# Kernel tuning notes

Measured on AMD Instinct MI355X. Metric: run time of the kernel, lower is better.

Reference implementation:

```python
import jax, jax.numpy as jnp
import numpy as np

N = 50000      # nodes
E = 800000     # edges
G = 512        # graphs
IN = 544; HID = 64; H = 4; OUT = 2
EPS = 1e-5

def setup_inputs():
    key = jax.random.key(0)
    ks = jax.random.split(key, 16)
    x = jax.random.normal(ks[0], (N, IN), jnp.float32)
    edge_index = jax.random.randint(ks[1], (2, E), 0, N, jnp.int64)
    batch = jnp.sort(jax.random.randint(ks[2], (N,), 0, G, jnp.int64))
    s = lambda k, shp, fan: jax.random.normal(k, shp, jnp.float32) / np.sqrt(fan)
    return {
        'x': x, 'edge_index': edge_index, 'batch': batch,
        'ln_g': jnp.ones((32,), jnp.float32), 'ln_b': jnp.zeros((32,), jnp.float32),
        'bn1_g': jnp.ones((512,), jnp.float32), 'bn1_b': jnp.zeros((512,), jnp.float32),
        'Wc': s(ks[3], (16, 512), 512), 'bc': jnp.zeros((16,), jnp.float32),
        'bn2_g': jnp.ones((48,), jnp.float32), 'bn2_b': jnp.zeros((48,), jnp.float32),
        'Wp': s(ks[4], (HID, 48), 48), 'bp': jnp.zeros((HID,), jnp.float32),
        'Wg': s(ks[5], (H * HID, HID), HID),
        'att_src': s(ks[6], (H, HID), HID), 'att_dst': s(ks[7], (H, HID), HID),
        'bg': jnp.zeros((H * HID,), jnp.float32),
        'bn3_g': jnp.ones((H * HID,), jnp.float32), 'bn3_b': jnp.zeros((H * HID,), jnp.float32),
        'W1': s(ks[8], (HID, H * HID), H * HID), 'b1': jnp.zeros((HID,), jnp.float32),
        'W2': s(ks[9], (OUT, HID), HID), 'b2': jnp.zeros((OUT,), jnp.float32),
    }

def _batchnorm(x, g, b):
    mu = jnp.mean(x, axis=0)
    var = jnp.var(x, axis=0)
    return (x - mu) * jax.lax.rsqrt(var + EPS) * g + b

def _forward(x, ln_g, ln_b, bn1_g, bn1_b, Wc, bc, bn2_g, bn2_b, Wp, bp,
             Wg, att_src, att_dst, bg, bn3_g, bn3_b, W1, b1, W2, b2,
             edge_index, batch):
    # feature split + norms
    x_cnn = _batchnorm(x[:, :512], bn1_g, bn1_b)
    f = x[:, 512:]
    mu = jnp.mean(f, axis=-1, keepdims=True)
    var = jnp.var(f, axis=-1, keepdims=True)
    f = (f - mu) * jax.lax.rsqrt(var + EPS) * ln_g + ln_b
    x_cnn = x_cnn @ Wc.T + bc                      # [N,16]
    z = jnp.concatenate([x_cnn, f], axis=1)        # [N,48]
    z = _batchnorm(z, bn2_g, bn2_b)
    z = jax.nn.relu(z @ Wp.T + bp)                 # [N,HID] (dropout=eval identity)
    # GATConv (concat=True, negative_slope=0.2)
    h = (z @ Wg.T).reshape(N, H, HID)              # [N,H,C]
    a_src = jnp.sum(h * att_src, axis=-1)          # [N,H]
    a_dst = jnp.sum(h * att_dst, axis=-1)          # [N,H]
    src, dst = edge_index[0], edge_index[1]
    e = jax.nn.leaky_relu(a_src[src] + a_dst[dst], 0.2)   # [E,H]
    m = jax.ops.segment_max(e, dst, num_segments=N)
    m = jnp.where(jnp.isfinite(m), m, 0.0)
    ex = jnp.exp(e - m[dst])
    s = jax.ops.segment_sum(ex, dst, num_segments=N)
    alpha = ex / jnp.maximum(s, 1e-16)[dst]               # [E,H]
    out = jax.ops.segment_sum(alpha[:, :, None] * h[src], dst, num_segments=N)
    out = out.reshape(N, H * HID) + bg
    # BatchNorm + ELU + mean pool + MLP head
    out = jax.nn.elu(_batchnorm(out, bn3_g, bn3_b))
    cnt = jax.ops.segment_sum(jnp.ones((N,), out.dtype), batch, num_segments=G)
    pooled = jax.ops.segment_sum(out, batch, num_segments=G) / jnp.maximum(cnt, 1.0)[:, None]
    hmlp = jax.nn.relu(pooled @ W1.T + b1)
    return hmlp @ W2.T + b2                        # [G,OUT]

def reference(x, edge_index, batch, ln_g, ln_b, bn1_g, bn1_b, Wc, bc, bn2_g, bn2_b,
              Wp, bp, Wg, att_src, att_dst, bg, bn3_g, bn3_b, W1, b1, W2, b2):
    return _forward(x, ln_g, ln_b, bn1_g, bn1_b, Wc, bc, bn2_g, bn2_b, Wp, bp,
                    Wg, att_src, att_dst, bg, bn3_g, bn3_b, W1, b1, W2, b2,
                    edge_index, batch)
```

## Files before the change

### kernel.cpp

```cpp
#include <hip/hip_runtime.h>

static constexpr int N_   = 50000;
static constexpr int E_   = 800000;
static constexpr int G_   = 512;
static constexpr int IN_  = 544;
static constexpr float EPS_ = 1e-5f;
static constexpr int NBLK = 782;

static constexpr int BN1C = 32;
static constexpr int BN3C = 16;
static constexpr int BN2C = 8;
static constexpr size_t OFF_BN1C   = 0;
static constexpr size_t OFF_BN2C   = 131072;
static constexpr size_t OFF_BN3C   = 134144;
static constexpr size_t ZERO_BYTES = 166912;
static constexpr size_t OFF_COUNT  = 166912;
static constexpr size_t OFF_OFFS   = 366912;
static constexpr size_t OFF_BH     = 566912;
static constexpr size_t OFF_BTOT   = 1367680;
static constexpr size_t OFF_BBASE  = 1368704;
static constexpr size_t OFF_SORTD  = 1369856;
static constexpr size_t OFF_SORTS  = 2969856;
static constexpr size_t OFF_SRCS   = 6169856;
static constexpr size_t OFF_WC2    = 9369856;
static constexpr size_t OFF_C2     = 9402624;
static constexpr size_t OFF_WP2    = 9402880;
static constexpr size_t OFF_CP     = 9415168;
static constexpr size_t OFF_WGT    = 9415424;
static constexpr size_t OFF_ASRC   = 9480960;
static constexpr size_t OFF_ADST   = 10280960;
static constexpr size_t OFF_Z      = 11080960;
static constexpr size_t OFF_H      = 20680960;
static constexpr size_t OFF_OUTP   = 46280960;

#define DEV static __device__ __forceinline__

DEV float lrelu(float v) { return v > 0.f ? v : 0.2f * v; }
DEV unsigned short f2bf(float f) {
    unsigned u = __float_as_uint(f);
    return (unsigned short)((u + 0x7fffu + ((u >> 16) & 1u)) >> 16);
}

__global__ __launch_bounds__(256) void k_bn1(
        const float* __restrict__ x, float* __restrict__ bn1c) {
    __shared__ float4 ta[256];
    __shared__ float4 tb[256];
    int t = threadIdx.x;
    int cq = t & 127, rsub = t >> 7;
    int c4 = cq << 2;
    float4 a = make_float4(0.f, 0.f, 0.f, 0.f);
    float4 b = make_float4(0.f, 0.f, 0.f, 0.f);
    for (int r = blockIdx.x * 2 + rsub; r < N_; r += gridDim.x * 2) {
        float4 v = *(const float4*)(x + (size_t)r * IN_ + c4);
        a.x += v.x; a.y += v.y; a.z += v.z; a.w += v.w;
        b.x += v.x * v.x; b.y += v.y * v.y; b.z += v.z * v.z; b.w += v.w * v.w;
    }
    ta[t] = a; tb[t] = b;
    __syncthreads();
    if (t < 128) {
        float4 sa = ta[t], sb = tb[t];
        float4 xa = ta[128 + t], xb = tb[128 + t];
        sa.x += xa.x; sa.y += xa.y; sa.z += xa.z; sa.w += xa.w;
        sb.x += xb.x; sb.y += xb.y; sb.z += xb.z; sb.w += xb.w;
        float* dst = bn1c + (size_t)(blockIdx.x & (BN1C - 1)) * 1024;
        int c = t << 2;
        atomicAdd(&dst[c + 0], sa.x); atomicAdd(&dst[c + 1], sa.y);
        atomicAdd(&dst[c + 2], sa.z); atomicAdd(&dst[c + 3], sa.w);
        atomicAdd(&dst[512 + c + 0], sb.x); atomicAdd(&dst[512 + c + 1], sb.y);
        atomicAdd(&dst[512 + c + 2], sb.z); atomicAdd(&dst[512 + c + 3], sb.w);
    }
}

__global__ __launch_bounds__(256) void k_rhist(
        const int* __restrict__ ei, int* __restrict__ blockhist) {
    __shared__ int hist[256];
    int t = threadIdx.x;
    hist[t] = 0;
    __syncthreads();
    int base = blockIdx.x * 1024;
#pragma unroll
    for (int k = 0; k < 4; k++) {
        int i = base + k * 256 + t;
        if (i < E_) atomicAdd(&hist[ei[E_ + i] >> 8], 1);
    }
    __syncthreads();
    blockhist[blockIdx.x * 256 + t] = hist[t];
}

__global__ __launch_bounds__(256) void k_rscan(
        int* __restrict__ blockhist, int* __restrict__ btot) {
    __shared__ int a[256];
    int b = blockIdx.x, t = threadIdx.x;
    int v[4]; int s = 0;
#pragma unroll
    for (int k = 0; k < 4; k++) {
        int j = t * 4 + k;
        v[k] = (j < NBLK) ? blockhist[j * 256 + b] : 0;
        s += v[k];
    }
    a[t] = s;
    for (int off = 1; off < 256; off <<= 1) {
        __syncthreads();
        int tmp = (t >= off) ? a[t - off] : 0;
        __syncthreads();
        a[t] += tmp;
    }
    __syncthreads();
    int run = a[t] - s;
#pragma unroll
    for (int k = 0; k < 4; k++) {
        int j = t * 4 + k;
        if (j < NBLK) { blockhist[j * 256 + b] = run; run += v[k]; }
    }
    if (t == 255) btot[b] = a[255];
}

__global__ __launch_bounds__(256) void k_rbase(
        const int* __restrict__ btot, int* __restrict__ bbase) {
    __shared__ int a[256];
    int t = threadIdx.x;
    int v = btot[t];
    a[t] = v;
    for (int off = 1; off < 256; off <<= 1) {
        __syncthreads();
        int tmp = (t >= off) ? a[t - off] : 0;
        __syncthreads();
        a[t] += tmp;
    }
    __syncthreads();
    bbase[t] = a[t] - v;
    if (t == 255) bbase[256] = a[255];
}

__global__ __launch_bounds__(256) void k_rscatter(
        const int* __restrict__ ei, const int* __restrict__ blockhist,
        const int* __restrict__ bbase, unsigned short* __restrict__ sortd,
        int* __restrict__ sorts) {
    __shared__ int cursor[256];
    int t = threadIdx.x;
    cursor[t] = bbase[t] + blockhist[blockIdx.x * 256 + t];
    __syncthreads();
    int base = blockIdx.x * 1024;
#pragma unroll
    for (int k = 0; k < 4; k++) {
        int i = base + k * 256 + t;
        if (i < E_) {
            int d = ei[E_ + i], s = ei[i];
            int pos = atomicAdd(&cursor[d >> 8], 1);
            sortd[pos] = (unsigned short)d;
            sorts[pos] = s;
        }
    }
}

__global__ __launch_bounds__(256) void k_rsort2(
        const unsigned short* __restrict__ sortd, const int* __restrict__ sorts,
        const int* __restrict__ bbase, int* __restrict__ count,
        int* __restrict__ offs, int* __restrict__ srcsort) {
    __shared__ int hist[256];
    __shared__ int pref[256];
    __shared__ int cursor[256];
    int b = blockIdx.x, t = threadIdx.x;
    int base = bbase[b], endp = bbase[b + 1];
    hist[t] = 0;
    __syncthreads();
    for (int i = base + t; i < endp; i += 256)
        atomicAdd(&hist[sortd[i] & 255], 1);
    __syncthreads();
    int hv = hist[t];
    pref[t] = hv;
    for (int off = 1; off < 256; off <<= 1) {
        __syncthreads();
        int tmp = (t >= off) ? pref[t - off] : 0;
        __syncthreads();
        pref[t] += tmp;
    }
    __syncthreads();
    int ex = pref[t] - hv;
    int idx = (b << 8) + t;
    if (idx < N_) { count[idx] = hv; offs[idx] = base + ex; }
    cursor[t] = ex;
    __syncthreads();
    for (int i = base + t; i < endp; i += 256) {
        int d = sortd[i], s = sorts[i];
        int pos = base + atomicAdd(&cursor[d & 255], 1);
        srcsort[pos] = s;
    }
}

__global__ __launch_bounds__(512) void k_fold1(
        const float* __restrict__ bn1c,
        const float* __restrict__ g, const float* __restrict__ b,
        const float* __restrict__ Wc, const float* __restrict__ bc,
        float* __restrict__ Wc2t, float* __restrict__ c2) {
    __shared__ float c2s[16];
    int j = threadIdx.x;
    if (j < 16) c2s[j] = 0.f;
    float sum = 0.f, sq = 0.f;
    for (int c = 0; c < BN1C; c++) {
        sum += bn1c[c * 1024 + j];
        sq  += bn1c[c * 1024 + 512 + j];
    }
    float mu  = sum / (float)N_;
    float var = sq / (float)N_ - mu * mu;
    float s   = g[j] * rsqrtf(var + EPS_);
    float tj  = b[j] - mu * s;
    __syncthreads();
    for (int i = 0; i < 16; i++) {
        float wv = Wc[i * 512 + j];
        Wc2t[i * 512 + j] = wv * s;
        float p = tj * wv;
        for (int m = 1; m < 64; m <<= 1) p += __shfl_xor(p, m);
        if ((j & 63) == 0) atomicAdd(&c2s[i], p);
    }
    __syncthreads();
    if (j < 16) c2[j] = c2s[j] + bc[j];
}

static constexpr int WSTRIDE = 516;
__global__ __launch_bounds__(512) void k_z(
        const float* __restrict__ x, const float* __restrict__ Wc2tg,
        const float* __restrict__ c2g, const float* __restrict__ lng,
        const float* __restrict__ lnb, float* __restrict__ z,
        float* __restrict__ bn2c) {
    __shared__ float wc2[16 * WSTRIDE];
    __shared__ float c2s[16];
    __shared__ float bsum[48];
    __shared__ float bsq[48];
    int t = threadIdx.x;
    for (int q = t; q < 8192; q += 512) {
        int row = q >> 9, col = q & 511;
        wc2[row * WSTRIDE + col] = Wc2tg[q];
    }
    if (t < 16) c2s[t] = c2g[t];
    if (t < 48) { bsum[t] = 0.f; bsq[t] = 0.f; }
    __syncthreads();
    int pr = t >> 3, i = t & 7;
    int n0 = blockIdx.x * 128 + pr * 2;
    int n1 = n0 + 1;
    bool v0 = n0 < N_, v1 = n1 < N_;
    const float4* xr0 = (const float4*)(x + (size_t)(v0 ? n0 : N_ - 1) * IN_);
    const float4* xr1 = (const float4*)(x + (size_t)(v1 ? n1 : N_ - 1) * IN_);
    const float4* w0 = (const float4*)(wc2 + i * WSTRIDE);
    const float4* w1 = (const float4*)(wc2 + (i + 8) * WSTRIDE);
    float a00 = c2s[i], a01 = c2s[i + 8];
    float a10 = a00, a11 = a01;
    for (int u = 0; u < 128; u++) {
        float4 xa = xr0[u], xb = xr1[u];
        float4 p = w0[u], q4 = w1[u];
        a00 += xa.x * p.x + xa.y * p.y + xa.z * p.z + xa.w * p.w;
        a01 += xa.x * q4.x + xa.y * q4.y + xa.z * q4.z + xa.w * q4.w;
        a10 += xb.x * p.x + xb.y * p.y + xb.z * p.z + xb.w * p.w;
        a11 += xb.x * q4.x + xb.y * q4.y + xb.z * q4.z + xb.w * q4.w;
    }
    float va[4], vb[4];
    float sm0 = 0.f, sq0 = 0.f, sm1 = 0.f, sq1 = 0.f;
#pragma unroll
    for (int jj = 0; jj < 4; jj++) {
        va[jj] = x[(size_t)(v0 ? n0 : N_ - 1) * IN_ + 512 + i + 8 * jj];
        vb[jj] = x[(size_t)(v1 ? n1 : N_ - 1) * IN_ + 512 + i + 8 * jj];
        sm0 += va[jj]; sq0 += va[jj] * va[jj];
        sm1 += vb[jj]; sq1 += vb[jj] * vb[jj];
    }
    for (int m = 1; m < 8; m <<= 1) {
        sm0 += __shfl_xor(sm0, m); sq0 += __shfl_xor(sq0, m);
        sm1 += __shfl_xor(sm1, m); sq1 += __shfl_xor(sq1, m);
    }
    float mu0 = sm0 * (1.f / 32.f), rs0 = rsqrtf(sq0 * (1.f / 32.f) - mu0 * mu0 + EPS_);
    float mu1 = sm1 * (1.f / 32.f), rs1 = rsqrtf(sq1 * (1.f / 32.f) - mu1 * mu1 + EPS_);
    float outa[6], outb[6];
    outa[0] = a00; outa[1] = a01; outb[0] = a10; outb[1] = a11;
#pragma unroll
    for (int jj = 0; jj < 4; jj++) {
        int c = i + 8 * jj;
        float gg = lng[c], bb = lnb[c];
        outa[2 + jj] = (va[jj] - mu0) * rs0 * gg + bb;
        outb[2 + jj] = (vb[jj] - mu1) * rs1 * gg + bb;
    }
    int cols[6] = { i, i + 8, 16 + i, 24 + i, 32 + i, 40 + i };
    if (v0) {
#pragma unroll
        for (int k = 0; k < 6; k++) z[n0 * 48 + cols[k]] = outa[k];
    }
    if (v1) {
#pragma unroll
        for (int k = 0; k < 6; k++) z[n1 * 48 + cols[k]] = outb[k];
    }
    float s6[6], q6[6];
#pragma unroll
    for (int k = 0; k < 6; k++) {
        float pa = v0 ? outa[k] : 0.f;
        float pb = v1 ? outb[k] : 0.f;
        s6[k] = pa + pb; q6[k] = pa * pa + pb * pb;
    }
#pragma unroll
    for (int m = 8; m < 64; m <<= 1) {
#pragma unroll
        for (int k = 0; k < 6; k++) {
            s6[k] += __shfl_xor(s6[k], m);
            q6[k] += __shfl_xor(q6[k], m);
        }
    }
    if ((t & 63) < 8) {
#pragma unroll
        for (int k = 0; k < 6; k++) {
            atomicAdd(&bsum[cols[k]], s6[k]);
            atomicAdd(&bsq[cols[k]],  q6[k]);
        }
    }
    __syncthreads();
    if (t < 48) {
        float* dst = bn2c + (size_t)(blockIdx.x & (BN2C - 1)) * 96;
        atomicAdd(&dst[t],      bsum[t]);
        atomicAdd(&dst[48 + t], bsq[t]);
    }
}

__global__ __launch_bounds__(256) void k_fold2_wgt(
        const float* __restrict__ bn2c,
        const float* __restrict__ g, const float* __restrict__ b,
        const float* __restrict__ Wp, const float* __restrict__ bp,
        float* __restrict__ Wp2, float* __restrict__ cp,
        const float* __restrict__ Wg, float* __restrict__ Wgt) {
    __shared__ float t2[48];
    int t = threadIdx.x;
    if (blockIdx.x > 0) {
        int idx = (blockIdx.x - 1) * 256 + t;
        int c = idx >> 6, k = idx & 63;
        Wgt[k * 256 + c] = Wg[idx];
        return;
    }
    if (t < 48) {
        float sum = 0.f, sq = 0.f;
        for (int c = 0; c < BN2C; c++) {
            sum += bn2c[c * 96 + t];
            sq  += bn2c[c * 96 + 48 + t];
        }
        float mu  = sum / (float)N_;
        float var = sq / (float)N_ - mu * mu;
        float s   = g[t] * rsqrtf(var + EPS_);
        t2[t] = b[t] - mu * s;
        for (int k = 0; k < 64; k++) Wp2[t * 64 + k] = Wp[k * 48 + t] * s;
    }
    __syncthreads();
    if (t < 64) {
        float acc = bp[t];
        for (int j = 0; j < 48; j++) acc += t2[j] * Wp[t * 48 + j];
        cp[t] = acc;
    }
}

__global__ __launch_bounds__(512) void k_h2(
        const float* __restrict__ z, const float* __restrict__ Wp2g,
        const float* __restrict__ cpg, const float* __restrict__ Wgtg,
        const float* __restrict__ att_s, const float* __restrict__ att_d,
        ushort4* __restrict__ hbf, float* __restrict__ asrc, float* __restrict__ adst) {
    __shared__ __align__(16) float4 wgh[32 * 64];
    __shared__ __align__(16) float  z1t[128 * 64];
    __shared__ __align__(16) float  wp2[48 * 64];
    __shared__ float  cps[64];
    __shared__ float4 ats[64];
    __shared__ float4 atd[64];
    int t = threadIdx.x;
    int base = blockIdx.x * 128;
    {
        const float4* z4 = (const float4*)(z + (size_t)base * 48);
        float4* zt4 = (float4*)wgh;
        for (int q = t; q < 1536; q += 512) zt4[q] = z4[q];
    }
    for (int q = t; q < 3072; q += 512) wp2[q] = Wp2g[q];
    if (t < 64) {
        cps[t] = cpg[t];
        ats[t] = ((const float4*)att_s)[t];
        atd[t] = ((const float4*)att_d)[t];
    }
    __syncthreads();
    int w = t >> 6, l = t & 63;
    {
        float wpr[48];
#pragma unroll
        for (int j = 0; j < 48; j++) wpr[j] = wp2[j * 64 + l];
        const float* zt = (const float*)wgh;
        for (int p = 0; p < 16; p++) {
            int nd = p * 8 + w;
            float acc = cps[l];
            const float4* zr4 = (const float4*)(zt + nd * 48);
#pragma unroll
            for (int u = 0; u < 12; u++) {
                float4 zv = zr4[u];
                acc += zv.x * wpr[u * 4 + 0] + zv.y * wpr[u * 4 + 1] +
                       zv.z * wpr[u * 4 + 2] + zv.w * wpr[u * 4 + 3];
            }
            z1t[nd * 64 + l] = fmaxf(acc, 0.f);
        }
    }
    const float4* wg4 = (const float4*)Wgtg;
    float4 acc[16];
#pragma unroll
    for (int nd = 0; nd < 16; nd++) acc[nd] = make_float4(0.f, 0.f, 0.f, 0.f);
    for (int half = 0; half < 2; half++) {
        __syncthreads();
        for (int q = t; q < 2048; q += 512) wgh[q] = wg4[half * 2048 + q];
        __syncthreads();
        int kbase = half * 32;
        for (int k4 = 0; k4 < 8; k4++) {
            float4 wv0 = wgh[(k4 * 4 + 0) * 64 + l];
            float4 wv1 = wgh[(k4 * 4 + 1) * 64 + l];
            float4 wv2 = wgh[(k4 * 4 + 2) * 64 + l];
            float4 wv3 = wgh[(k4 * 4 + 3) * 64 + l];
#pragma unroll
            for (int nd = 0; nd < 16; nd++) {
                float4 zv = *(const float4*)&z1t[(w * 16 + nd) * 64 + kbase + k4 * 4];
                acc[nd].x += zv.x * wv0.x + zv.y * wv1.x + zv.z * wv2.x + zv.w * wv3.x;
                acc[nd].y += zv.x * wv0.y + zv.y * wv1.y + zv.z * wv2.y + zv.w * wv3.y;
                acc[nd].z += zv.x * wv0.z + zv.y * wv1.z + zv.z * wv2.z + zv.w * wv3.z;
                acc[nd].w += zv.x * wv0.w + zv.y * wv1.w + zv.z * wv2.w + zv.w * wv3.w;
            }
        }
    }
    float4 as4 = ats[l], ad4 = atd[l];
#pragma unroll
    for (int nd = 0; nd < 16; nd++) {
        int node = base + w * 16 + nd;
        if (node < N_) {
            ushort4 hv;
            hv.x = f2bf(acc[nd].x); hv.y = f2bf(acc[nd].y);
            hv.z = f2bf(acc[nd].z); hv.w = f2bf(acc[nd].w);
            hbf[(size_t)node * 64 + l] = hv;
            float pa = acc[nd].x * as4.x + acc[nd].y * as4.y +
                       acc[nd].z * as4.z + acc[nd].w * as4.w;
            float pb = acc[nd].x * ad4.x + acc[nd].y * ad4.y +
                       acc[nd].z * ad4.z + acc[nd].w * ad4.w;
            for (int m = 1; m < 16; m <<= 1) {
                pa += __shfl_xor(pa, m);
                pb += __shfl_xor(pb, m);
            }
            if ((l & 15) == 0) {
                asrc[node * 4 + (l >> 4)] = pa;
                adst[node * 4 + (l >> 4)] = pb;
            }
        }
    }
}

__global__ __launch_bounds__(256) void k_agg(
        const int* __restrict__ count, const int* __restrict__ offs,
        const int* __restrict__ srcsort, const float* __restrict__ asrc,
        const float* __restrict__ adst, const ushort4* __restrict__ hbf,
        const float* __restrict__ bg, ushort4* __restrict__ outbf) {
    __shared__ int   s_src[4][128];
    __shared__ float s_wf[4][512];
    int w = threadIdx.x >> 6, l = threadIdx.x & 63;
    int dst = blockIdx.x * 4 + w;
    const float4* asrc4 = (const float4*)asrc;
    float4 bgv = ((const float4*)bg)[l];
    int deg = count[dst];
    if (deg == 0) {
        ushort4 o;
        o.x = f2bf(bgv.x); o.y = f2bf(bgv.y); o.z = f2bf(bgv.z); o.w = f2bf(bgv.w);
        outbf[(size_t)dst * 64 + l] = o;
        return;
    }
    int base = offs[dst];
    float4 ad = ((const float4*)adst)[dst];
    const float NEGINF = -__builtin_inff();
    float4 e0 = make_float4(NEGINF, NEGINF, NEGINF, NEGINF);
    float4 e1 = make_float4(NEGINF, NEGINF, NEGINF, NEGINF);
    if (l < deg) {
        int s0 = srcsort[base + l];
        s_src[w][l] = s0;
        float4 a = asrc4[s0];
        e0 = make_float4(lrelu(a.x + ad.x), lrelu(a.y + ad.y),
                         lrelu(a.z + ad.z), lrelu(a.w + ad.w));
    }
    if (l + 64 < deg) {
        int s1 = srcsort[base + l + 64];
        s_src[w][l + 64] = s1;
        float4 a = asrc4[s1];
        e1 = make_float4(lrelu(a.x + ad.x), lrelu(a.y + ad.y),
                         lrelu(a.z + ad.z), lrelu(a.w + ad.w));
    }
    float4 mx = make_float4(fmaxf(e0.x, e1.x), fmaxf(e0.y, e1.y),
                            fmaxf(e0.z, e1.z), fmaxf(e0.w, e1.w));
    for (int j = l + 128; j < deg; j += 64) {
        int s2 = srcsort[base + j];
        float4 a = asrc4[s2];
        mx.x = fmaxf(mx.x, lrelu(a.x + ad.x)); mx.y = fmaxf(mx.y, lrelu(a.y + ad.y));
        mx.z = fmaxf(mx.z, lrelu(a.z + ad.z)); mx.w = fmaxf(mx.w, lrelu(a.w + ad.w));
    }
    for (int m = 1; m < 64; m <<= 1) {
        mx.x = fmaxf(mx.x, __shfl_xor(mx.x, m));
        mx.y = fmaxf(mx.y, __shfl_xor(mx.y, m));
        mx.z = fmaxf(mx.z, __shfl_xor(mx.z, m));
        mx.w = fmaxf(mx.w, __shfl_xor(mx.w, m));
    }
    float4 sv = make_float4(0.f, 0.f, 0.f, 0.f);
    if (l < deg) {
        float4 ex = make_float4(__expf(e0.x - mx.x), __expf(e0.y - mx.y),
                                __expf(e0.z - mx.z), __expf(e0.w - mx.w));
        *(float4*)&s_wf[w][l * 4] = ex;
        sv.x += ex.x; sv.y += ex.y; sv.z += ex.z; sv.w += ex.w;
    }
    if (l + 64 < deg) {
        float4 ex = make_float4(__expf(e1.x - mx.x), __expf(e1.y - mx.y),
                                __expf(e1.z - mx.z), __expf(e1.w - mx.w));
        *(float4*)&s_wf[w][(l + 64) * 4] = ex;
        sv.x += ex.x; sv.y += ex.y; sv.z += ex.z; sv.w += ex.w;
    }
    for (int j = l + 128; j < deg; j += 64) {
        int s2 = srcsort[base + j];
        float4 a = asrc4[s2];
        sv.x += __expf(lrelu(a.x + ad.x) - mx.x);
        sv.y += __expf(lrelu(a.y + ad.y) - mx.y);
        sv.z += __expf(lrelu(a.z + ad.z) - mx.z);
        sv.w += __expf(lrelu(a.w + ad.w) - mx.w);
    }
    for (int m = 1; m < 64; m <<= 1) {
        sv.x += __shfl_xor(sv.x, m); sv.y += __shfl_xor(sv.y, m);
        sv.z += __shfl_xor(sv.z, m); sv.w += __shfl_xor(sv.w, m);
    }
    int hd = l >> 4;
    float mh  = hd == 0 ? mx.x : hd == 1 ? mx.y : hd == 2 ? mx.z : mx.w;
    float sh  = hd == 0 ? sv.x : hd == 1 ? sv.y : hd == 2 ? sv.z : sv.w;
    float adh = hd == 0 ? ad.x : hd == 1 ? ad.y : hd == 2 ? ad.z : ad.w;
    float inv = 1.f / fmaxf(sh, 1e-16f);
    float4 accv = make_float4(0.f, 0.f, 0.f, 0.f);
    const uint2* h2p = (const uint2*)hbf;
    int dcap = deg < 128 ? deg : 128;
#pragma unroll 2
    for (int j = 0; j < dcap; j++) {
        int src = s_src[w][j];
        float wgt = s_wf[w][j * 4 + hd] * inv;
        uint2 u = h2p[(size_t)src * 64 + l];
        accv.x += wgt * __uint_as_float(u.x << 16);
        accv.y += wgt * __uint_as_float(u.x & 0xffff0000u);
        accv.z += wgt * __uint_as_float(u.y << 16);
        accv.w += wgt * __uint_as_float(u.y & 0xffff0000u);
    }
    for (int j = 128; j < deg; j++) {
        int src = srcsort[base + j];
        float4 a = asrc4[src];
        float ah = hd == 0 ? a.x : hd == 1 ? a.y : hd == 2 ? a.z : a.w;
        float wgt = __expf(lrelu(ah + adh) - mh) * inv;
        uint2 u = h2p[(size_t)src * 64 + l];
        accv.x += wgt * __uint_as_float(u.x << 16);
        accv.y += wgt * __uint_as_float(u.x & 0xffff0000u);
        accv.z += wgt * __uint_as_float(u.y << 16);
        accv.w += wgt * __uint_as_float(u.y & 0xffff0000u);
    }
    ushort4 o;
    o.x = f2bf(accv.x + bgv.x); o.y = f2bf(accv.y + bgv.y);
    o.z = f2bf(accv.z + bgv.z); o.w = f2bf(accv.w + bgv.w);
    outbf[(size_t)dst * 64 + l] = o;
}

__global__ __launch_bounds__(256) void k_bn3_stats(
        const uint2* __restrict__ op2, float* __restrict__ bn3c) {
    __shared__ float4 ta[256];
    __shared__ float4 tb[256];
    int t = threadIdx.x;
    int cq = t & 63, rsub = t >> 6;
    float4 a = make_float4(0.f, 0.f, 0.f, 0.f);
    float4 b = make_float4(0.f, 0.f, 0.f, 0.f);
    for (int r = blockIdx.x * 4 + rsub; r < N_; r += gridDim.x * 4) {
        uint2 u = op2[(size_t)r * 64 + cq];
        float x0 = __uint_as_float(u.x << 16);
        float x1 = __uint_as_float(u.x & 0xffff0000u);
        float x2 = __uint_as_float(u.y << 16);
        float x3 = __uint_as_float(u.y & 0xffff0000u);
        a.x += x0; a.y += x1; a.z += x2; a.w += x3;
        b.x += x0 * x0; b.y += x1 * x1; b.z += x2 * x2; b.w += x3 * x3;
    }
    ta[t] = a; tb[t] = b;
    __syncthreads();
    if (t < 64) {
        float4 sa = ta[t], sb = tb[t];
#pragma unroll
        for (int r = 1; r < 4; r++) {
            float4 xa = ta[r * 64 + t], xb = tb[r * 64 + t];
            sa.x += xa.x; sa.y += xa.y; sa.z += xa.z; sa.w += xa.w;
            sb.x += xb.x; sb.y += xb.y; sb.z += xb.z; sb.w += xb.w;
        }
        float* dst = bn3c + (size_t)(blockIdx.x & (BN3C - 1)) * 512;
        int c = t << 2;
        atomicAdd(&dst[c + 0], sa.x); atomicAdd(&dst[c + 1], sa.y);
        atomicAdd(&dst[c + 2], sa.z); atomicAdd(&dst[c + 3], sa.w);
        atomicAdd(&dst[256 + c + 0], sb.x); atomicAdd(&dst[256 + c + 1], sb.y);
        atomicAdd(&dst[256 + c + 2], sb.z); atomicAdd(&dst[256 + c + 3], sb.w);
    }
}

__global__ __launch_bounds__(256) void k_pool_mlp(
        const uint2* __restrict__ op2, const int* __restrict__ batch,
        const float* __restrict__ bn3c,
        const float* __restrict__ bn3g, const float* __restrict__ bn3b,
        const float* __restrict__ W1, const float* __restrict__ b1,
        const float* __restrict__ W2, const float* __restrict__ b2,
        float* __restrict__ out) {
    __shared__ float4 tile[256];
    __shared__ float  pl[256];
    __shared__ float  hm[64];
    __shared__ float  s3[256];
    __shared__ float  q3[256];
    int g = blockIdx.x;
    int t = threadIdx.x;
    int cq = t & 63, rsub = t >> 6;
    int c4 = cq << 2;
    {
        float s = 0.f, q = 0.f;
        for (int c = 0; c < BN3C; c++) {
            s += bn3c[c * 512 + t];
            q += bn3c[c * 512 + 256 + t];
        }
        s3[t] = s; q3[t] = q;
    }
    int lo = 0, hi = N_;
    while (lo < hi) { int mid = (lo + hi) >> 1; if (batch[mid] < g) lo = mid + 1; else hi = mid; }
    int start = lo;
    hi = N_;
    while (lo < hi) { int mid = (lo + hi) >> 1; if (batch[mid] < g + 1) lo = mid + 1; else hi = mid; }
    int end = lo;
    __syncthreads();
    float scv[4], shv[4];
#pragma unroll
    for (int k = 0; k < 4; k++) {
        int c = c4 + k;
        float mu  = s3[c] / (float)N_;
        float var = q3[c] / (float)N_ - mu * mu;
        float s   = bn3g[c] * rsqrtf(var + EPS_);
        scv[k] = s; shv[k] = bn3b[c] - mu * s;
    }
    float4 acc = make_float4(0.f, 0.f, 0.f, 0.f);
    for (int n = start + rsub; n < end; n += 4) {
        uint2 u = op2[(size_t)n * 64 + cq];
        float e0 = __uint_as_float(u.x << 16)          * scv[0] + shv[0];
        float e1 = __uint_as_float(u.x & 0xffff0000u)  * scv[1] + shv[1];
        float e2 = __uint_as_float(u.y << 16)          * scv[2] + shv[2];
        float e3 = __uint_as_float(u.y & 0xffff0000u)  * scv[3] + shv[3];
        acc.x += (e0 > 0.f) ? e0 : expm1f(e0);
        acc.y += (e1 > 0.f) ? e1 : expm1f(e1);
        acc.z += (e2 > 0.f) ? e2 : expm1f(e2);
        acc.w += (e3 > 0.f) ? e3 : expm1f(e3);
    }
    tile[t] = acc;
    __syncthreads();
    if (t < 64) {
        float4 s = tile[t];
#pragma unroll
        for (int r = 1; r < 4; r++) {
            float4 xv = tile[r * 64 + t];
            s.x += xv.x; s.y += xv.y; s.z += xv.z; s.w += xv.w;
        }
        float icn = 1.f / fmaxf((float)(end - start), 1.f);
        ((float4*)pl)[t] = make_float4(s.x * icn, s.y * icn, s.z * icn, s.w * icn);
    }
    __syncthreads();
    {
        int j = t >> 2, part = t & 3;
        const float* w1r = W1 + j * 256 + part * 64;
        const float* plr = pl + part * 64;
        float a = 0.f;
#pragma unroll
        for (int c = 0; c < 64; c++) a += w1r[c] * plr[c];
        a += __shfl_xor(a, 1);
        a += __shfl_xor(a, 2);
        if (part == 0) hm[j] = fmaxf(a + b1[j], 0.f);
    }
    __syncthreads();
    if (t < 128) {
        int j = t >> 6, k = t & 63;
        float p = W2[j * 64 + k] * hm[k];
        for (int m = 1; m < 64; m <<= 1) p += __shfl_xor(p, m);
        if (k == 0) out[g * 2 + j] = p + b2[j];
    }
}

extern "C" void kernel_launch(void* const* d_in, const int* in_sizes, int n_in,
                              void* d_out, int out_size, void* d_ws, size_t ws_size,
                              hipStream_t stream) {
    const float* x    = (const float*)d_in[0];
    const int*   ei   = (const int*)d_in[1];
    const int*   batch= (const int*)d_in[2];
    const float* lng  = (const float*)d_in[3];
    const float* lnb  = (const float*)d_in[4];
    const float* bn1g = (const float*)d_in[5];
    const float* bn1b = (const float*)d_in[6];
    const float* Wc   = (const float*)d_in[7];
    const float* bc   = (const float*)d_in[8];
    const float* bn2g = (const float*)d_in[9];
    const float* bn2b = (const float*)d_in[10];
    const float* Wp   = (const float*)d_in[11];
    const float* bp   = (const float*)d_in[12];
    const float* Wg   = (const float*)d_in[13];
    const float* atts = (const float*)d_in[14];
    const float* attd = (const float*)d_in[15];
    const float* bg   = (const float*)d_in[16];
    const float* bn3g = (const float*)d_in[17];
    const float* bn3b = (const float*)d_in[18];
    const float* W1   = (const float*)d_in[19];
    const float* b1   = (const float*)d_in[20];
    const float* W2   = (const float*)d_in[21];
    const float* b2   = (const float*)d_in[22];
    float* out = (float*)d_out;

    char* w8 = (char*)d_ws;
    float* bn1c   = (float*)(w8 + OFF_BN1C);
    float* bn2c   = (float*)(w8 + OFF_BN2C);
    float* bn3c   = (float*)(w8 + OFF_BN3C);
    int*   count  = (int*)(w8 + OFF_COUNT);
    int*   offs   = (int*)(w8 + OFF_OFFS);
    int*   bh     = (int*)(w8 + OFF_BH);
    int*   btot   = (int*)(w8 + OFF_BTOT);
    int*   bbase  = (int*)(w8 + OFF_BBASE);
    unsigned short* sortd = (unsigned short*)(w8 + OFF_SORTD);
    int*   sorts  = (int*)(w8 + OFF_SORTS);
    int*   srcs   = (int*)(w8 + OFF_SRCS);
    float* Wc2t   = (float*)(w8 + OFF_WC2);
    float* c2     = (float*)(w8 + OFF_C2);
    float* Wp2    = (float*)(w8 + OFF_WP2);
    float* cp     = (float*)(w8 + OFF_CP);
    float* Wgt    = (float*)(w8 + OFF_WGT);
    float* asrc   = (float*)(w8 + OFF_ASRC);
    float* adst   = (float*)(w8 + OFF_ADST);
    float* z      = (float*)(w8 + OFF_Z);
    ushort4* hbf  = (ushort4*)(w8 + OFF_H);
    ushort4* outp = (ushort4*)(w8 + OFF_OUTP);

    hipMemsetAsync(d_ws, 0, ZERO_BYTES, stream);

    k_bn1<<<2048, 256, 0, stream>>>(x, bn1c);
    k_rhist<<<NBLK, 256, 0, stream>>>(ei, bh);
    k_fold1<<<1, 512, 0, stream>>>(bn1c, bn1g, bn1b, Wc, bc, Wc2t, c2);
    k_rscan<<<256, 256, 0, stream>>>(bh, btot);
    k_z<<<(N_ + 127) / 128, 512, 0, stream>>>(x, Wc2t, c2, lng, lnb, z, bn2c);
    k_rbase<<<1, 256, 0, stream>>>(btot, bbase);
    k_rscatter<<<NBLK, 256, 0, stream>>>(ei, bh, bbase, sortd, sorts);
    k_fold2_wgt<<<65, 256, 0, stream>>>(bn2c, bn2g, bn2b, Wp, bp, Wp2, cp, Wg, Wgt);
    k_rsort2<<<196, 256, 0, stream>>>(sortd, sorts, bbase, count, offs, srcs);
    k_h2<<<(N_ + 127) / 128, 512, 0, stream>>>(z, Wp2, cp, Wgt, atts, attd, hbf, asrc, adst);
    k_agg<<<N_ / 4, 256, 0, stream>>>(count, offs, srcs, asrc, adst, hbf, bg, outp);
    k_bn3_stats<<<1024, 256, 0, stream>>>((const uint2*)outp, bn3c);
    k_pool_mlp<<<G_, 256, 0, stream>>>((const uint2*)outp, batch, bn3c,
                                       bn3g, bn3b, W1, b1, W2, b2, out);
}
```

Before: 519.4 us.

## Halve k_h2 tile, fold attention vectors into Wg, pad z1 shared rows

```diff
diff --git a/kernel.cpp b/kernel.cpp
--- a/kernel.cpp
+++ b/kernel.cpp
@@ -27,11 +27,12 @@
 static constexpr size_t OFF_WP2    = 9402880;
 static constexpr size_t OFF_CP     = 9415168;
 static constexpr size_t OFF_WGT    = 9415424;
-static constexpr size_t OFF_ASRC   = 9480960;
-static constexpr size_t OFF_ADST   = 10280960;
-static constexpr size_t OFF_Z      = 11080960;
-static constexpr size_t OFF_H      = 20680960;
-static constexpr size_t OFF_OUTP   = 46280960;
+static constexpr size_t OFF_AF     = 9480960;
+static constexpr size_t OFF_ASRC   = 9483008;
+static constexpr size_t OFF_ADST   = 10283008;
+static constexpr size_t OFF_Z      = 11083008;
+static constexpr size_t OFF_H      = 20683008;
+static constexpr size_t OFF_OUTP   = 46283008;
 
 #define DEV static __device__ __forceinline__
 
@@ -321,11 +322,26 @@
         const float* __restrict__ g, const float* __restrict__ b,
         const float* __restrict__ Wp, const float* __restrict__ bp,
         float* __restrict__ Wp2, float* __restrict__ cp,
-        const float* __restrict__ Wg, float* __restrict__ Wgt) {
+        const float* __restrict__ Wg, float* __restrict__ Wgt,
+        const float* __restrict__ att_s, const float* __restrict__ att_d,
+        float* __restrict__ afold) {
     __shared__ float t2[48];
     int t = threadIdx.x;
-    if (blockIdx.x > 0) {
-        int idx = (blockIdx.x - 1) * 256 + t;
+    int bid = blockIdx.x;
+    if (bid == 65) {
+        int head = t >> 6, k = t & 63;
+        float as = 0.f, ad = 0.f;
+        for (int c = 0; c < 64; c++) {
+            float wv = Wg[(head * 64 + c) * 64 + k];
+            as += att_s[head * 64 + c] * wv;
+            ad += att_d[head * 64 + c] * wv;
+        }
+        afold[t] = as;
+        afold[256 + t] = ad;
+        return;
+    }
+    if (bid > 0) {
+        int idx = (bid - 1) * 256 + t;
         int c = idx >> 6, k = idx & 63;
         Wgt[k * 256 + c] = Wg[idx];
         return;
@@ -350,67 +366,67 @@
     }
 }
 
-__global__ __launch_bounds__(512) void k_h2(
+static constexpr int Z1S = 68;
+__global__ __launch_bounds__(512, 6) void k_h2(
         const float* __restrict__ z, const float* __restrict__ Wp2g,
         const float* __restrict__ cpg, const float* __restrict__ Wgtg,
-        const float* __restrict__ att_s, const float* __restrict__ att_d,
+        const float* __restrict__ afg,
         ushort4* __restrict__ hbf, float* __restrict__ asrc, float* __restrict__ adst) {
-    __shared__ __align__(16) float4 wgh[32 * 64];
-    __shared__ __align__(16) float  z1t[128 * 64];
+    __shared__ __align__(16) float4 wgh[16 * 64];
+    __shared__ __align__(16) float  z1t[64 * Z1S];
     __shared__ __align__(16) float  wp2[48 * 64];
+    __shared__ __align__(16) float  afs[8 * Z1S];
     __shared__ float  cps[64];
-    __shared__ float4 ats[64];
-    __shared__ float4 atd[64];
-    int t = threadIdx.x;
-    int base = blockIdx.x * 128;
+    int t = threadIdx.x;
+    int base = blockIdx.x * 64;
     {
         const float4* z4 = (const float4*)(z + (size_t)base * 48);
         float4* zt4 = (float4*)wgh;
-        for (int q = t; q < 1536; q += 512) zt4[q] = z4[q];
+        for (int q = t; q < 768; q += 512) zt4[q] = z4[q];
     }
     for (int q = t; q < 3072; q += 512) wp2[q] = Wp2g[q];
-    if (t < 64) {
-        cps[t] = cpg[t];
-        ats[t] = ((const float4*)att_s)[t];
-        atd[t] = ((const float4*)att_d)[t];
-    }
+    if (t < 512) { int row = t >> 6, k = t & 63; afs[row * Z1S + k] = afg[t]; }
+    if (t < 64) cps[t] = cpg[t];
     __syncthreads();
     int w = t >> 6, l = t & 63;
     {
-        float wpr[48];
-#pragma unroll
-        for (int j = 0; j < 48; j++) wpr[j] = wp2[j * 64 + l];
+        float acc1[8];
+#pragma unroll
+        for (int nd = 0; nd < 8; nd++) acc1[nd] = cps[l];
         const float* zt = (const float*)wgh;
-        for (int p = 0; p < 16; p++) {
-            int nd = p * 8 + w;
-            float acc = cps[l];
-            const float4* zr4 = (const float4*)(zt + nd * 48);
-#pragma unroll
-            for (int u = 0; u < 12; u++) {
-                float4 zv = zr4[u];
-                acc += zv.x * wpr[u * 4 + 0] + zv.y * wpr[u * 4 + 1] +
-                       zv.z * wpr[u * 4 + 2] + zv.w * wpr[u * 4 + 3];
+        for (int u = 0; u < 12; u++) {
+            float p0 = wp2[(u * 4 + 0) * 64 + l];
+            float p1 = wp2[(u * 4 + 1) * 64 + l];
+            float p2 = wp2[(u * 4 + 2) * 64 + l];
+            float p3 = wp2[(u * 4 + 3) * 64 + l];
+#pragma unroll
+            for (int nd = 0; nd < 8; nd++) {
+                float4 zv = ((const float4*)(zt + (w * 8 + nd) * 48))[u];
+                acc1[nd] += zv.x * p0 + zv.y * p1 + zv.z * p2 + zv.w * p3;
             }
-            z1t[nd * 64 + l] = fmaxf(acc, 0.f);
-        }
+        }
+#pragma unroll
+        for (int nd = 0; nd < 8; nd++)
+            z1t[(w * 8 + nd) * Z1S + l] = fmaxf(acc1[nd], 0.f);
     }
     const float4* wg4 = (const float4*)Wgtg;
-    float4 acc[16];
-#pragma unroll
-    for (int nd = 0; nd < 16; nd++) acc[nd] = make_float4(0.f, 0.f, 0.f, 0.f);
-    for (int half = 0; half < 2; half++) {
+    float4 acc[8];
+#pragma unroll
+    for (int nd = 0; nd < 8; nd++) acc[nd] = make_float4(0.f, 0.f, 0.f, 0.f);
+    for (int chunk = 0; chunk < 4; chunk++) {
         __syncthreads();
-        for (int q = t; q < 2048; q += 512) wgh[q] = wg4[half * 2048 + q];
+        for (int q = t; q < 1024; q += 512) wgh[q] = wg4[chunk * 1024 + q];
         __syncthreads();
-        int kbase = half * 32;
-        for (int k4 = 0; k4 < 8; k4++) {
+        int kbase = chunk * 16;
+#pragma unroll
+        for (int k4 = 0; k4 < 4; k4++) {
             float4 wv0 = wgh[(k4 * 4 + 0) * 64 + l];
             float4 wv1 = wgh[(k4 * 4 + 1) * 64 + l];
             float4 wv2 = wgh[(k4 * 4 + 2) * 64 + l];
             float4 wv3 = wgh[(k4 * 4 + 3) * 64 + l];
 #pragma unroll
-            for (int nd = 0; nd < 16; nd++) {
-                float4 zv = *(const float4*)&z1t[(w * 16 + nd) * 64 + kbase + k4 * 4];
+            for (int nd = 0; nd < 8; nd++) {
+                float4 zv = *(const float4*)&z1t[(w * 8 + nd) * Z1S + kbase + k4 * 4];
                 acc[nd].x += zv.x * wv0.x + zv.y * wv1.x + zv.z * wv2.x + zv.w * wv3.x;
                 acc[nd].y += zv.x * wv0.y + zv.y * wv1.y + zv.z * wv2.y + zv.w * wv3.y;
                 acc[nd].z += zv.x * wv0.z + zv.y * wv1.z + zv.z * wv2.z + zv.w * wv3.z;
@@ -418,27 +434,31 @@
             }
         }
     }
-    float4 as4 = ats[l], ad4 = atd[l];
-#pragma unroll
-    for (int nd = 0; nd < 16; nd++) {
-        int node = base + w * 16 + nd;
+#pragma unroll
+    for (int nd = 0; nd < 8; nd++) {
+        int node = base + w * 8 + nd;
         if (node < N_) {
             ushort4 hv;
             hv.x = f2bf(acc[nd].x); hv.y = f2bf(acc[nd].y);
             hv.z = f2bf(acc[nd].z); hv.w = f2bf(acc[nd].w);
             hbf[(size_t)node * 64 + l] = hv;
-            float pa = acc[nd].x * as4.x + acc[nd].y * as4.y +
-                       acc[nd].z * as4.z + acc[nd].w * as4.w;
-            float pb = acc[nd].x * ad4.x + acc[nd].y * ad4.y +
-                       acc[nd].z * ad4.z + acc[nd].w * ad4.w;
-            for (int m = 1; m < 16; m <<= 1) {
-                pa += __shfl_xor(pa, m);
-                pb += __shfl_xor(pb, m);
-            }
-            if ((l & 15) == 0) {
-                asrc[node * 4 + (l >> 4)] = pa;
-                adst[node * 4 + (l >> 4)] = pb;
-            }
+        }
+    }
+    {
+        int node = t >> 3, q = t & 7;
+        int head = q >> 1, sd = q & 1;
+        const float4* zr = (const float4*)&z1t[node * Z1S];
+        const float4* ar = (const float4*)&afs[(sd * 4 + head) * Z1S];
+        float a = 0.f;
+#pragma unroll
+        for (int u = 0; u < 16; u++) {
+            float4 z4 = zr[u], a4 = ar[u];
+            a += z4.x * a4.x + z4.y * a4.y + z4.z * a4.z + z4.w * a4.w;
+        }
+        int gn = base + node;
+        if (gn < N_) {
+            float* dst = sd ? adst : asrc;
+            dst[gn * 4 + head] = a;
         }
     }
 }
@@ -720,6 +740,7 @@
     float* Wp2    = (float*)(w8 + OFF_WP2);
     float* cp     = (float*)(w8 + OFF_CP);
     float* Wgt    = (float*)(w8 + OFF_WGT);
+    float* afold  = (float*)(w8 + OFF_AF);
     float* asrc   = (float*)(w8 + OFF_ASRC);
     float* adst   = (float*)(w8 + OFF_ADST);
     float* z      = (float*)(w8 + OFF_Z);
@@ -735,9 +756,10 @@
     k_z<<<(N_ + 127) / 128, 512, 0, stream>>>(x, Wc2t, c2, lng, lnb, z, bn2c);
     k_rbase<<<1, 256, 0, stream>>>(btot, bbase);
     k_rscatter<<<NBLK, 256, 0, stream>>>(ei, bh, bbase, sortd, sorts);
-    k_fold2_wgt<<<65, 256, 0, stream>>>(bn2c, bn2g, bn2b, Wp, bp, Wp2, cp, Wg, Wgt);
+    k_fold2_wgt<<<66, 256, 0, stream>>>(bn2c, bn2g, bn2b, Wp, bp, Wp2, cp, Wg, Wgt,
+                                        atts, attd, afold);
     k_rsort2<<<196, 256, 0, stream>>>(sortd, sorts, bbase, count, offs, srcs);
-    k_h2<<<(N_ + 127) / 128, 512, 0, stream>>>(z, Wp2, cp, Wgt, atts, attd, hbf, asrc, adst);
+    k_h2<<<(N_ + 63) / 64, 512, 0, stream>>>(z, Wp2, cp, Wgt, afold, hbf, asrc, adst);
     k_agg<<<N_ / 4, 256, 0, stream>>>(count, offs, srcs, asrc, adst, hbf, bg, outp);
     k_bn3_stats<<<1024, 256, 0, stream>>>((const uint2*)outp, bn3c);
     k_pool_mlp<<<G_, 256, 0, stream>>>((const uint2*)outp, batch, bn3c,
```

New measurement: 699.5 us. 34.7% more time.
